# Performance work log

Measured on AMD Instinct MI355X. Metric: run time of the kernel, lower is better.

Reference implementation:

```python
import jax, jax.numpy as jnp
import numpy as np

D = 256; H = 8; HD = D // H; NK = 32; NLAYERS = 4; FF = 4 * D
B = 8; M = 768; N = 128; LT = 64; T = M + N + LT
SCALE = 1.0 / float(np.sqrt(HD))


def layer_norm(x, s, b):
    mu = x.mean(-1, keepdims=True)
    var = ((x - mu) ** 2).mean(-1, keepdims=True)
    return (x - mu) * jax.lax.rsqrt(var + 1e-5) * s + b


def sine_embed(pos, d):
    # MTR gen_sineembed_for_position: half dims for y, half for x, interleaved sin/cos
    half = d // 2
    dim_t = jnp.power(10000.0, 2.0 * (jnp.arange(half) // 2).astype(jnp.float32) / half)
    scale = 2.0 * np.pi
    def inter(e):
        return jnp.stack([jnp.sin(e[:, 0::2]), jnp.cos(e[:, 1::2])], -1).reshape(e.shape[0], -1)
    ex = pos[:, 0:1] * scale / dim_t
    ey = pos[:, 1:2] * scale / dim_t
    return jnp.concatenate([inter(ey), inter(ex)], -1)


def setup_inputs() -> dict:
    key = jax.random.key(0)
    ks = jax.random.split(key, 24)
    s = 0.02
    inp = {
        'map_token': jax.random.normal(ks[0], (B, M, D), jnp.float32),
        'agent_token': jax.random.normal(ks[1], (B, N, D), jnp.float32),
        'light_token': jax.random.normal(ks[2], (B, LT, D), jnp.float32),
        'map_position': jax.random.uniform(ks[3], (B, M, 2), jnp.float32) * 100.0,
        'agent_position': jax.random.uniform(ks[4], (B, N, 2), jnp.float32) * 100.0,
        'light_position': jax.random.uniform(ks[5], (B, LT, 2), jnp.float32) * 100.0,
        'map_valid_mask': jnp.ones((B, M), bool),
        'agent_valid_mask': jnp.ones((B, N), bool),
        'light_valid_mask': jnp.ones((B, LT), bool),
        'Wq': jax.random.normal(ks[6], (NLAYERS, D, D), jnp.float32) * s,
        'bq': jnp.zeros((NLAYERS, D), jnp.float32),
        'Wk': jax.random.normal(ks[7], (NLAYERS, D, D), jnp.float32) * s,
        'bk': jnp.zeros((NLAYERS, D), jnp.float32),
        'Wv': jax.random.normal(ks[8], (NLAYERS, D, D), jnp.float32) * s,
        'bv': jnp.zeros((NLAYERS, D), jnp.float32),
        'Wo': jax.random.normal(ks[9], (NLAYERS, D, D), jnp.float32) * s,
        'bo': jnp.zeros((NLAYERS, D), jnp.float32),
        'W1': jax.random.normal(ks[10], (NLAYERS, D, FF), jnp.float32) * s,
        'b1': jnp.zeros((NLAYERS, FF), jnp.float32),
        'W2': jax.random.normal(ks[11], (NLAYERS, FF, D), jnp.float32) * s,
        'b2': jnp.zeros((NLAYERS, D), jnp.float32),
        'ln1_s': jnp.ones((NLAYERS, D), jnp.float32),
        'ln1_b': jnp.zeros((NLAYERS, D), jnp.float32),
        'ln2_s': jnp.ones((NLAYERS, D), jnp.float32),
        'ln2_b': jnp.zeros((NLAYERS, D), jnp.float32),
    }
    return inp


def reference(map_token, agent_token, light_token, map_position, agent_position, light_position,
              map_valid_mask, agent_valid_mask, light_valid_mask,
              Wq, bq, Wk, bk, Wv, bv, Wo, bo, W1, b1, W2, b2, ln1_s, ln1_b, ln2_s, ln2_b):
    x = jnp.concatenate([map_token, agent_token, light_token], 1)             # [B,T,D]
    pos = jnp.concatenate([map_position, agent_position, light_position], 1)[..., :2]  # [B,T,2]
    # all tokens valid -> masked compaction is a static reshape
    xs = x.reshape(B * T, D)
    ps = pos.reshape(B * T, 2)
    # KNN within each scene (includes self, like knn_batch_mlogk on same set)
    d2 = jnp.sum((pos[:, :, None, :] - pos[:, None, :, :]) ** 2, -1)          # [B,T,T]
    _, idx = jax.lax.top_k(-d2, NK)                                            # [B,T,NK] local indices
    idx = (idx + (jnp.arange(B) * T)[:, None, None]).reshape(B * T, NK)        # global flat indices
    pe = sine_embed(ps, D)                                                     # [B*T,D]
    out = xs
    for l in range(NLAYERS):
        qk = out + pe
        q = (qk @ Wq[l] + bq[l]).reshape(-1, H, HD)
        k = (qk @ Wk[l] + bk[l]).reshape(-1, H, HD)
        v = (out @ Wv[l] + bv[l]).reshape(-1, H, HD)
        kn = k[idx]                                                            # [BT,NK,H,HD] gather
        vn = v[idx]
        att = jax.nn.softmax(jnp.einsum('nhd,nkhd->nhk', q, kn) * SCALE, axis=-1)
        a = jnp.einsum('nhk,nkhd->nhd', att, vn).reshape(-1, D) @ Wo[l] + bo[l]
        out = layer_norm(out + a, ln1_s[l], ln1_b[l])
        ff = jax.nn.relu(out @ W1[l] + b1[l]) @ W2[l] + b2[l]
        out = layer_norm(out + ff, ln2_s[l], ln2_b[l])
    full = out.reshape(B, T, D)
    return full[:, :M], full[:, M:M + N], full[:, M + N:]
```

## Files before the change

kernel.cpp:

```cpp
#include <hip/hip_runtime.h>
#include <math.h>

#define BB 8
#define MTOK 768
#define NTOK 128
#define LTOK 64
#define TT 960
#define BT 7680
#define DD 256
#define HH 8
#define HD 32
#define KNN 32
#define FFD 1024
#define NLAYERS 4
#define SCALE_ATT 0.17677669529663687f

typedef __attribute__((ext_vector_type(8))) short bfrag_t;
typedef __attribute__((ext_vector_type(4))) float accfrag_t;

__device__ __forceinline__ float b2f(unsigned short u) {
  union { unsigned int i; float f; } c; c.i = ((unsigned int)u) << 16; return c.f;
}
__device__ __forceinline__ unsigned short f2b(float f) {
  union { float f; unsigned int i; } c; c.f = f;
  return (unsigned short)((c.i + 0x7fffu + ((c.i >> 16) & 1u)) >> 16);
}
__device__ __forceinline__ float load_elem(const void* p, size_t i, int f) {
  return f ? b2f(((const unsigned short*)p)[i]) : ((const float*)p)[i];
}
__device__ __forceinline__ size_t pk_addr(int row, int col, int nks) {
  return ((size_t)((row >> 4) * nks + (col >> 5)) << 9)
       + (size_t)(((((col >> 3) & 3) << 4) + (row & 15)) * 8 + (col & 7));
}
__device__ __forceinline__ int swiz_tok(int blk) { return (blk & 7) * TT + (blk >> 3); }

__global__ __launch_bounds__(256)
void detect_kernel(const void* tok, int* flag) {
  __shared__ int cnt;
  if (threadIdx.x == 0) cnt = 0;
  __syncthreads();
  const unsigned short* u = (const unsigned short*)tok;
  int ok = 0;
  for (int i = threadIdx.x; i < 1024; i += 256) {
    int e = (u[i] >> 7) & 0xFF;
    if (e >= 100 && e <= 140) ok++;
  }
  atomicAdd(&cnt, ok);
  __syncthreads();
  if (threadIdx.x == 0) *flag = (cnt >= 922) ? 1 : 0;
}

#define FB_BQ 0
#define FB_BK 1024
#define FB_BV 2048
#define FB_BO 3072
#define FB_B1 4096
#define FB_B2 8192
#define FB_LN1S 9216
#define FB_LN1B 10240
#define FB_LN2S 11264
#define FB_LN2B 12288
#define FB_TOTAL 13312
struct ParamSrc { const void* p[13]; };
__global__ __launch_bounds__(256)
void conv_misc_kernel(ParamSrc ps, const int* flag, float* __restrict__ dst,
                      float* __restrict__ posf) {
  int f = *flag;
  if (blockIdx.x < BB) {
    int b = blockIdx.x;
    for (int t = threadIdx.x; t < TT * 2; t += 256) {
      int tok = t >> 1, c = t & 1;
      const void* p; size_t idx;
      if (tok < MTOK)             { p = ps.p[10]; idx = (size_t)(b * MTOK + tok) * 2 + c; }
      else if (tok < MTOK + NTOK) { p = ps.p[11]; idx = (size_t)(b * NTOK + tok - MTOK) * 2 + c; }
      else                        { p = ps.p[12]; idx = (size_t)(b * LTOK + tok - MTOK - NTOK) * 2 + c; }
      posf[((size_t)b * TT + tok) * 2 + c] = load_elem(p, idx, f);
    }
    return;
  }
  int i = (blockIdx.x - BB) * 256 + threadIdx.x;
  if (i >= FB_TOTAL) return;
  int src; size_t off;
  if (i < 4096)      { src = i >> 10;              off = i & 1023; }
  else if (i < 8192) { src = 4;                    off = i - 4096; }
  else               { src = 5 + ((i - 8192) >> 10); off = (i - 8192) & 1023; }
  dst[i] = load_elem(ps.p[src], off, f);
}

struct PackSrc { const void* s[6]; };
__global__ __launch_bounds__(256)
void packW_kernel(PackSrc w, const int* flag,
                  unsigned short* __restrict__ Wqkvpk, unsigned short* __restrict__ Wopk,
                  unsigned short* __restrict__ W1pk, unsigned short* __restrict__ W2pk) {
  int f = *flag;
  int id = blockIdx.x * 256 + threadIdx.x;
  const void* src; unsigned short* dst; int layer, e, K, N;
  if (id < 786432) {
    layer = id / 196608; int rest = id % 196608; int sel = rest / 65536; e = rest % 65536;
    src = w.s[sel]; dst = Wqkvpk + id; K = 256; N = 256;
  } else if (id < 1048576) {
    int off = id - 786432; layer = off / 65536; e = off % 65536;
    src = w.s[3]; dst = Wopk + off; K = 256; N = 256;
  } else if (id < 2097152) {
    int off = id - 1048576; layer = off / 262144; e = off % 262144;
    src = w.s[4]; dst = W1pk + off; K = 256; N = 1024;
  } else {
    int off = id - 2097152; layer = off / 262144; e = off % 262144;
    src = w.s[5]; dst = W2pk + off; K = 1024; N = 256;
  }
  int nks = K >> 5;
  int cb = e / (nks * 512);
  int ks = (e / 512) % nks;
  int lane = (e >> 3) & 63, j = e & 7;
  int col = cb * 16 + (lane & 15);
  int k = ks * 32 + (lane >> 4) * 8 + j;
  size_t si = (size_t)layer * K * N + (size_t)k * N + col;
  *dst = f ? ((const unsigned short*)src)[si] : f2b(((const float*)src)[si]);
}

__global__ __launch_bounds__(256)
void prep_kernel(const void* mt, const void* at, const void* lt,
                 const float* __restrict__ posf, const int* flag,
                 unsigned short* __restrict__ pe_b, float* __restrict__ out_f,
                 unsigned short* __restrict__ pk1, unsigned short* __restrict__ qkpk) {
  int n = swiz_tok(blockIdx.x), d = threadIdx.x;
  int b = n / TT, t = n - b * TT;
  int f = *flag;
  const void* src; size_t si;
  if (t < MTOK)              { src = mt; si = (size_t)(b * MTOK + t) * DD + d; }
  else if (t < MTOK + NTOK)  { src = at; si = (size_t)(b * NTOK + (t - MTOK)) * DD + d; }
  else                       { src = lt; si = (size_t)(b * LTOK + (t - MTOK - NTOK)) * DD + d; }
  float x = load_elem(src, si, f);
  float px = posf[((size_t)b * TT + t) * 2 + 0];
  float py = posf[((size_t)b * TT + t) * 2 + 1];
  float coord = (d < 128) ? py : px;
  int j = d & 127;
  float expo = (float)(2 * (j >> 1)) / 128.0f;
  float dim_t = powf(10000.0f, expo);
  float e = coord * 6.283185307179586f / dim_t;
  float p = (j & 1) ? cosf(e) : sinf(e);
  size_t o = (size_t)n * DD + d;
  pe_b[o] = f2b(p);
  out_f[o] = x;
  size_t pa = pk_addr(n, d, 8);
  pk1[pa] = f2b(x);
  qkpk[pa] = f2b(x + p);
}

__device__ __forceinline__ unsigned long long shfl_xor_u64(unsigned long long v, int m) {
  unsigned lo = (unsigned)v, hi = (unsigned)(v >> 32);
  lo = (unsigned)__shfl_xor((int)lo, m);
  hi = (unsigned)__shfl_xor((int)hi, m);
  return ((unsigned long long)hi << 32) | (unsigned long long)lo;
}
__device__ __forceinline__ unsigned long long shfl_u64(unsigned long long v, int srcLane) {
  unsigned lo = (unsigned)v, hi = (unsigned)(v >> 32);
  lo = (unsigned)__shfl((int)lo, srcLane);
  hi = (unsigned)__shfl((int)hi, srcLane);
  return ((unsigned long long)hi << 32) | (unsigned long long)lo;
}
__device__ __forceinline__ unsigned long long bitonic64(unsigned long long key, int lane) {
#pragma unroll
  for (int kk = 2; kk <= 64; kk <<= 1) {
#pragma unroll
    for (int j = kk >> 1; j > 0; j >>= 1) {
      unsigned long long other = shfl_xor_u64(key, j);
      bool small_ = (lane & j) == 0;
      bool dir = (lane & kk) == 0;
      bool keep = ((key < other) == (small_ == dir));
      key = keep ? key : other;
    }
  }
  return key;
}

__global__ __launch_bounds__(256)
void knn_kernel(const float* __restrict__ posf, int* __restrict__ idx_out) {
  __shared__ float sx[TT], sy[TT];
  __shared__ unsigned long long cbuf[4][64];
  int b = blockIdx.x & 7;
  int qbase = (blockIdx.x >> 3) * 4;
  for (int t = threadIdx.x; t < TT; t += 256) {
    sx[t] = posf[((size_t)b * TT + t) * 2 + 0];
    sy[t] = posf[((size_t)b * TT + t) * 2 + 1];
  }
  __syncthreads();
  int wave = threadIdx.x >> 6, lane = threadIdx.x & 63;
  int t = qbase + wave;
  float qx = sx[t], qy = sy[t];

  unsigned long long k[15];
#pragma unroll
  for (int c = 0; c < 15; c++) {
    int j = c * 64 + lane;
    float dx = qx - sx[j], dy = qy - sy[j];
    float d2 = __fadd_rn(__fmul_rn(dx, dx), __fmul_rn(dy, dy));
    k[c] = ((unsigned long long)__float_as_uint(d2) << 32) | (unsigned)j;
  }
  unsigned long long lm = k[0];
#pragma unroll
  for (int c = 1; c < 15; c++) lm = (k[c] < lm) ? k[c] : lm;

  unsigned long long sm = bitonic64(lm, lane);
  unsigned long long thr = shfl_u64(sm, 31);

  int c_l = 0;
#pragma unroll
  for (int c = 0; c < 15; c++) c_l += (k[c] <= thr) ? 1 : 0;
  int inc = c_l;
#pragma unroll
  for (int o = 1; o < 64; o <<= 1) {
    int tt = __shfl_up(inc, o);
    inc += (lane >= o) ? tt : 0;
  }
  int total = __shfl(inc, 63);
  int pos = inc - c_l;

  if (total <= 64) {
    unsigned long long* wb = cbuf[wave];
#pragma unroll
    for (int c = 0; c < 15; c++) {
      if (k[c] <= thr) { wb[pos] = k[c]; pos++; }
    }
    unsigned long long cand = (lane < total) ? wb[lane] : ~0ull;
    cand = bitonic64(cand, lane);
    if (lane < KNN)
      idx_out[((size_t)(b * TT + t)) * KNN + lane] = b * TT + (int)(cand & 0xFFFFFFFFu);
  } else {
    unsigned res = 0;
    for (int i = 0; i < KNN; i++) {
      unsigned long long m = k[0];
#pragma unroll
      for (int c = 1; c < 15; c++) m = (k[c] < m) ? k[c] : m;
#pragma unroll
      for (int o = 32; o > 0; o >>= 1) {
        unsigned long long om = shfl_xor_u64(m, o);
        m = (om < m) ? om : m;
      }
      if (lane == i) res = (unsigned)(m & 0xFFFFFFFFu);
      int owner = (int)(m & 63u), ch = (int)(((unsigned)(m & 0xFFFFFFFFu)) >> 6);
      if (lane == owner) {
#pragma unroll
        for (int c = 0; c < 15; c++) if (c == ch) k[c] = ~0ull;
      }
    }
    if (lane < KNN)
      idx_out[((size_t)(b * TT + t)) * KNN + lane] = b * TT + (int)res;
  }
}

template<int NKS>
__device__ __forceinline__ void wavegemm(const unsigned short* __restrict__ Apk,
                                         const unsigned short* __restrict__ Bpk,
                                         int rb, int cb0, accfrag_t (&acc)[4]) {
  const int lane = threadIdx.x & 63;
  accfrag_t z = {0.f, 0.f, 0.f, 0.f};
#pragma unroll
  for (int nt = 0; nt < 4; nt++) acc[nt] = z;
  const unsigned short* ap = Apk + ((size_t)rb * NKS * 512 + lane * 8);
  const unsigned short* bp = Bpk + ((size_t)cb0 * NKS * 512 + lane * 8);
#pragma unroll 4
  for (int ks = 0; ks < NKS; ks++) {
    bfrag_t a = *(const bfrag_t*)(ap + ks * 512);
#pragma unroll
    for (int nt = 0; nt < 4; nt++) {
      bfrag_t b = *(const bfrag_t*)(bp + (size_t)(nt * NKS + ks) * 512);
      acc[nt] = __builtin_amdgcn_mfma_f32_16x16x32_bf16(a, b, acc[nt], 0, 0, 0);
    }
  }
}

__global__ __launch_bounds__(256)
void qkv_kernel(const unsigned short* __restrict__ qkpk,
                const unsigned short* __restrict__ outpk,
                const unsigned short* __restrict__ Wl,
                const float* __restrict__ pb, int l,
                unsigned short* __restrict__ QKV) {
  int scene = blockIdx.x & 7, r = blockIdx.x >> 3;
  int rbg = r % 15, cgall = r / 15;
  int wave = threadIdx.x >> 6, lane = threadIdx.x & 63;
  int rb = scene * 60 + rbg * 4 + wave;
  int sel = cgall >> 2, cg = cgall & 3;
  const unsigned short* A = (sel < 2) ? qkpk : outpk;
  const unsigned short* B = Wl + sel * 65536;
  const float* bias = pb + sel * 1024 + l * 256;
  accfrag_t acc[4];
  wavegemm<8>(A, B, rb, cg * 4, acc);
  int l16 = lane & 15, lq = lane >> 4;
  unsigned short* C = QKV + (size_t)sel * BT * DD;
#pragma unroll
  for (int nt = 0; nt < 4; nt++) {
    int col = cg * 64 + nt * 16 + l16;
    float bv = bias[col];
#pragma unroll
    for (int r4 = 0; r4 < 4; r4++) {
      int row = rb * 16 + lq * 4 + r4;
      C[(size_t)row * DD + col] = f2b(acc[nt][r4] + bv);
    }
  }
}

__global__ __launch_bounds__(256)
void attn_kernel(const unsigned short* __restrict__ QKV,
                 const int* __restrict__ idx,
                 unsigned short* __restrict__ attnpk) {
  __shared__ unsigned short kn[KNN][DD + 8];
  __shared__ unsigned short vn[KNN][DD + 8];
  __shared__ float qs[DD];
  __shared__ float att[HH][KNN];
  __shared__ int nb[KNN];
  const unsigned short* Q = QKV;
  const unsigned short* K = QKV + (size_t)BT * DD;
  const unsigned short* V = QKV + 2 * (size_t)BT * DD;
  int n = swiz_tok(blockIdx.x), tid = threadIdx.x;
  if (tid < KNN) nb[tid] = idx[n * KNN + tid];
  qs[tid] = b2f(Q[(size_t)n * DD + tid]);
  __syncthreads();
#pragma unroll
  for (int p = 0; p < 4; p++) {
    int e = p * 256 + tid;
    int r = e >> 5, c8 = (e & 31) * 8;
    int srow = nb[r];
    *(uint4*)(&kn[r][c8]) = *(const uint4*)(K + (size_t)srow * DD + c8);
    *(uint4*)(&vn[r][c8]) = *(const uint4*)(V + (size_t)srow * DD + c8);
  }
  __syncthreads();
  int h = tid >> 5, kk = tid & 31;
  float dot = 0.0f;
#pragma unroll
  for (int d = 0; d < HD; d++) dot += qs[h * HD + d] * b2f(kn[kk][h * HD + d]);
  float sc = dot * SCALE_ATT;
  float mx = sc;
#pragma unroll
  for (int o = 16; o > 0; o >>= 1) mx = fmaxf(mx, __shfl_xor(mx, o, 32));
  float ex = expf(sc - mx);
  float sm = ex;
#pragma unroll
  for (int o = 16; o > 0; o >>= 1) sm += __shfl_xor(sm, o, 32);
  att[h][kk] = ex / sm;
  __syncthreads();
  int d = kk;
  float oacc = 0.0f;
#pragma unroll
  for (int k2 = 0; k2 < KNN; k2++) oacc += att[h][k2] * b2f(vn[k2][h * HD + d]);
  attnpk[pk_addr(n, tid, 8)] = f2b(oacc);
}

template<bool LAST>
__global__ __launch_bounds__(256)
void ffn_block_kernel(const unsigned short* __restrict__ attnpk,
                      const unsigned short* __restrict__ Wo,
                      const unsigned short* __restrict__ W1,
                      const unsigned short* __restrict__ W2,
                      const float* __restrict__ bo,
                      const float* __restrict__ b1,
                      const float* __restrict__ b2,
                      float* __restrict__ yf,
                      unsigned short* __restrict__ outpk, unsigned short* __restrict__ qkpk,
                      const unsigned short* __restrict__ pe_b,
                      const float* __restrict__ g1, const float* __restrict__ t1,
                      const float* __restrict__ g2, const float* __restrict__ t2,
                      void* __restrict__ dout, const int* __restrict__ flag) {
  __shared__ unsigned short xls[8 * 512];
  __shared__ unsigned short hls[32 * 512];
  __shared__ float ps1[4][16], ps2[4][16];
  int scene = blockIdx.x & 7, rbs = blockIdx.x >> 3;
  int wave = threadIdx.x >> 6, lane = threadIdx.x & 63;
  int rb = scene * 60 + rbs;
  int l16 = lane & 15, lq = lane >> 4;

  accfrag_t acc[4];
  wavegemm<8>(attnpk, Wo, rb, wave * 4, acc);
  float y[4][4];
  float s[4] = {0.f, 0.f, 0.f, 0.f}, s2[4] = {0.f, 0.f, 0.f, 0.f};
#pragma unroll
  for (int nt = 0; nt < 4; nt++) {
    int col = wave * 64 + nt * 16 + l16;
    float bv = bo[col];
#pragma unroll
    for (int r4 = 0; r4 < 4; r4++) {
      int row = rb * 16 + lq * 4 + r4;
      float x = acc[nt][r4] + bv + yf[(size_t)row * DD + col];
      y[nt][r4] = x; s[r4] += x; s2[r4] += x * x;
    }
  }
#pragma unroll
  for (int o = 1; o < 16; o <<= 1) {
#pragma unroll
    for (int r4 = 0; r4 < 4; r4++) { s[r4] += __shfl_xor(s[r4], o); s2[r4] += __shfl_xor(s2[r4], o); }
  }
  if (l16 == 0) {
#pragma unroll
    for (int r4 = 0; r4 < 4; r4++) { ps1[wave][lq * 4 + r4] = s[r4]; ps2[wave][lq * 4 + r4] = s2[r4]; }
  }
  __syncthreads();
#pragma unroll
  for (int r4 = 0; r4 < 4; r4++) {
    int r16 = lq * 4 + r4;
    float ts  = ps1[0][r16] + ps1[1][r16] + ps1[2][r16] + ps1[3][r16];
    float ts2 = ps2[0][r16] + ps2[1][r16] + ps2[2][r16] + ps2[3][r16];
    float mu = ts * (1.0f / 256.0f);
    float var = ts2 * (1.0f / 256.0f) - mu * mu;
    float rstd = 1.0f / sqrtf(fmaxf(var, 0.f) + 1e-5f);
#pragma unroll
    for (int nt = 0; nt < 4; nt++) {
      int col = wave * 64 + nt * 16 + l16;
      float v = (y[nt][r4] - mu) * rstd * g1[col] + t1[col];
      y[nt][r4] = v;
      xls[pk_addr(r16, col, 8)] = f2b(v);
    }
  }
  __syncthreads();

#pragma unroll
  for (int i = 0; i < 4; i++) {
    int cg = wave * 4 + i;
    accfrag_t a2[4];
    wavegemm<8>(xls, W1, 0, cg * 4, a2);
#pragma unroll
    for (int nt = 0; nt < 4; nt++) {
      int col = cg * 64 + nt * 16 + l16;
      float bv = b1[col];
#pragma unroll
      for (int r4 = 0; r4 < 4; r4++)
        hls[pk_addr(lq * 4 + r4, col, 32)] = f2b(fmaxf(a2[nt][r4] + bv, 0.0f));
    }
  }
  __syncthreads();

  accfrag_t a3[4];
  wavegemm<32>(hls, W2, 0, wave * 4, a3);
  float v2[4][4];
  float s3[4] = {0.f, 0.f, 0.f, 0.f}, s4[4] = {0.f, 0.f, 0.f, 0.f};
#pragma unroll
  for (int nt = 0; nt < 4; nt++) {
    int col = wave * 64 + nt * 16 + l16;
    float bv = b2[col];
#pragma unroll
    for (int r4 = 0; r4 < 4; r4++) {
      float x = a3[nt][r4] + bv + y[nt][r4];
      v2[nt][r4] = x; s3[r4] += x; s4[r4] += x * x;
    }
  }
#pragma unroll
  for (int o = 1; o < 16; o <<= 1) {
#pragma unroll
    for (int r4 = 0; r4 < 4; r4++) { s3[r4] += __shfl_xor(s3[r4], o); s4[r4] += __shfl_xor(s4[r4], o); }
  }
  if (l16 == 0) {
#pragma unroll
    for (int r4 = 0; r4 < 4; r4++) { ps1[wave][lq * 4 + r4] = s3[r4]; ps2[wave][lq * 4 + r4] = s4[r4]; }
  }
  __syncthreads();
  int fl = LAST ? *flag : 0;
#pragma unroll
  for (int r4 = 0; r4 < 4; r4++) {
    int r16 = lq * 4 + r4;
    float ts  = ps1[0][r16] + ps1[1][r16] + ps1[2][r16] + ps1[3][r16];
    float ts2 = ps2[0][r16] + ps2[1][r16] + ps2[2][r16] + ps2[3][r16];
    float mu = ts * (1.0f / 256.0f);
    float var = ts2 * (1.0f / 256.0f) - mu * mu;
    float rstd = 1.0f / sqrtf(fmaxf(var, 0.f) + 1e-5f);
#pragma unroll
    for (int nt = 0; nt < 4; nt++) {
      int col = wave * 64 + nt * 16 + l16;
      float yv = (v2[nt][r4] - mu) * rstd * g2[col] + t2[col];
      int row = rb * 16 + r16;
      if (!LAST) {
        yf[(size_t)row * DD + col] = yv;
        outpk[pk_addr(row, col, 8)] = f2b(yv);
        float q = yv + b2f(pe_b[(size_t)row * DD + col]);
        qkpk[pk_addr(row, col, 8)] = f2b(q);
      } else {
        int t = rbs * 16 + r16;
        size_t o;
        if (t < MTOK)             o = (size_t)(scene * MTOK + t) * DD + col;
        else if (t < MTOK + NTOK) o = (size_t)BB * MTOK * DD + (size_t)(scene * NTOK + (t - MTOK)) * DD + col;
        else                      o = (size_t)BB * MTOK * DD + (size_t)BB * NTOK * DD
                                    + (size_t)(scene * LTOK + (t - MTOK - NTOK)) * DD + col;
        if (fl) ((unsigned short*)dout)[o] = f2b(yv);
        else    ((float*)dout)[o] = yv;
      }
    }
  }
}

extern "C" void kernel_launch(void* const* d_in, const int* in_sizes, int n_in,
                              void* d_out, int out_size, void* d_ws, size_t ws_size,
                              hipStream_t stream) {
  const void* map_tok   = d_in[0];
  const void* agent_tok = d_in[1];
  const void* light_tok = d_in[2];
  const void* map_pos   = d_in[3];
  const void* agent_pos = d_in[4];
  const void* light_pos = d_in[5];
  const void* Wq  = d_in[9];
  const void* bq  = d_in[10];
  const void* Wk  = d_in[11];
  const void* bk  = d_in[12];
  const void* Wv  = d_in[13];
  const void* bv  = d_in[14];
  const void* Wo  = d_in[15];
  const void* bo  = d_in[16];
  const void* W1  = d_in[17];
  const void* b1  = d_in[18];
  const void* W2  = d_in[19];
  const void* b2  = d_in[20];
  const void* ln1s = d_in[21];
  const void* ln1b = d_in[22];
  const void* ln2s = d_in[23];
  const void* ln2b = d_in[24];

  size_t off = 0;
  char* base = (char*)d_ws;
  auto take = [&](size_t bytes) { char* p = base + off; off += (bytes + 255) & ~(size_t)255; return (void*)p; };
  int*   flag  = (int*)take(256);
  float* posf  = (float*)take((size_t)BT * 2 * 4);
  float* pbuf  = (float*)take((size_t)FB_TOTAL * 4);
  unsigned short* pe_b = (unsigned short*)take((size_t)BT * DD * 2);
  float* out_f = (float*)take((size_t)BT * DD * 4);
  unsigned short* pk1  = (unsigned short*)take((size_t)BT * DD * 2);
  unsigned short* qkpk = (unsigned short*)take((size_t)BT * DD * 2);
  unsigned short* QKV  = (unsigned short*)take((size_t)3 * BT * DD * 2);
  unsigned short* attnpk = (unsigned short*)take((size_t)BT * DD * 2);
  int* idxb = (int*)take((size_t)BT * KNN * 4);
  unsigned short* Wqkvpk = (unsigned short*)take((size_t)NLAYERS * 3 * DD * DD * 2);
  unsigned short* Wopk   = (unsigned short*)take((size_t)NLAYERS * DD * DD * 2);
  unsigned short* W1pk   = (unsigned short*)take((size_t)NLAYERS * DD * FFD * 2);
  unsigned short* W2pk   = (unsigned short*)take((size_t)NLAYERS * DD * FFD * 2);

  detect_kernel<<<1, 256, 0, stream>>>(map_tok, flag);
  ParamSrc ps; ps.p[0]=bq; ps.p[1]=bk; ps.p[2]=bv; ps.p[3]=bo; ps.p[4]=b1;
  ps.p[5]=b2; ps.p[6]=ln1s; ps.p[7]=ln1b; ps.p[8]=ln2s; ps.p[9]=ln2b;
  ps.p[10]=map_pos; ps.p[11]=agent_pos; ps.p[12]=light_pos;
  conv_misc_kernel<<<BB + (FB_TOTAL + 255) / 256, 256, 0, stream>>>(ps, flag, pbuf, posf);

  PackSrc pw; pw.s[0]=Wq; pw.s[1]=Wk; pw.s[2]=Wv; pw.s[3]=Wo; pw.s[4]=W1; pw.s[5]=W2;
  packW_kernel<<<12288, 256, 0, stream>>>(pw, flag, Wqkvpk, Wopk, W1pk, W2pk);

  prep_kernel<<<BT, 256, 0, stream>>>(map_tok, agent_tok, light_tok, posf, flag,
                                      pe_b, out_f, pk1, qkpk);
  knn_kernel<<<1920, 256, 0, stream>>>(posf, idxb);

  for (int l = 0; l < NLAYERS; l++) {
    qkv_kernel<<<1440, 256, 0, stream>>>(qkpk, pk1, Wqkvpk + (size_t)l * 3 * 65536,
                                         pbuf, l, QKV);
    attn_kernel<<<BT, 256, 0, stream>>>(QKV, idxb, attnpk);
    if (l < NLAYERS - 1)
      ffn_block_kernel<false><<<480, 256, 0, stream>>>(
          attnpk, Wopk + (size_t)l * 65536, W1pk + (size_t)l * 262144, W2pk + (size_t)l * 262144,
          pbuf + FB_BO + l * 256, pbuf + FB_B1 + l * 1024, pbuf + FB_B2 + l * 256,
          out_f, pk1, qkpk, pe_b,
          pbuf + FB_LN1S + l * 256, pbuf + FB_LN1B + l * 256,
          pbuf + FB_LN2S + l * 256, pbuf + FB_LN2B + l * 256,
          d_out, flag);
    else
      ffn_block_kernel<true><<<480, 256, 0, stream>>>(
          attnpk, Wopk + (size_t)l * 65536, W1pk + (size_t)l * 262144, W2pk + (size_t)l * 262144,
          pbuf + FB_BO + l * 256, pbuf + FB_B1 + l * 1024, pbuf + FB_B2 + l * 256,
          out_f, pk1, qkpk, pe_b,
          pbuf + FB_LN1S + l * 256, pbuf + FB_LN1B + l * 256,
          pbuf + FB_LN2S + l * 256, pbuf + FB_LN2B + l * 256,
          d_out, flag);
  }
}
```

Baseline: 429.9 us.

## Fuse next-layer QKV projection into FFN block and merge setup kernels

Folds the detect step into conv_misc and merges packW, prep and knn into one launch using block-index ranges. Weight packing now reads the source coalesced and scatters into the packed layout. The FFN block keeps its normalized output tile in shared memory and computes the next layer's Q/K/V projection in place. This removes the separate per-layer qkv launch and the round trip of pk1/qkpk through global memory. The cost is more per-block work and shared-memory reuse in the FFN kernel, which may lower occupancy.

```diff
diff --git a/kernel.cpp b/kernel.cpp
--- a/kernel.cpp
+++ b/kernel.cpp
@@ -34,22 +34,6 @@
 }
 __device__ __forceinline__ int swiz_tok(int blk) { return (blk & 7) * TT + (blk >> 3); }
 
-__global__ __launch_bounds__(256)
-void detect_kernel(const void* tok, int* flag) {
-  __shared__ int cnt;
-  if (threadIdx.x == 0) cnt = 0;
-  __syncthreads();
-  const unsigned short* u = (const unsigned short*)tok;
-  int ok = 0;
-  for (int i = threadIdx.x; i < 1024; i += 256) {
-    int e = (u[i] >> 7) & 0xFF;
-    if (e >= 100 && e <= 140) ok++;
-  }
-  atomicAdd(&cnt, ok);
-  __syncthreads();
-  if (threadIdx.x == 0) *flag = (cnt >= 922) ? 1 : 0;
-}
-
 #define FB_BQ 0
 #define FB_BK 1024
 #define FB_BV 2048
@@ -63,18 +47,30 @@
 #define FB_TOTAL 13312
 struct ParamSrc { const void* p[13]; };
 __global__ __launch_bounds__(256)
-void conv_misc_kernel(ParamSrc ps, const int* flag, float* __restrict__ dst,
-                      float* __restrict__ posf) {
-  int f = *flag;
+void conv_misc_kernel(ParamSrc ps, const void* tok, int* flagout,
+                      float* __restrict__ dst, float* __restrict__ posf) {
+  __shared__ int cnt;
+  if (threadIdx.x == 0) cnt = 0;
+  __syncthreads();
+  const unsigned short* u = (const unsigned short*)tok;
+  int ok = 0;
+  for (int i = threadIdx.x; i < 1024; i += 256) {
+    int e = (u[i] >> 7) & 0xFF;
+    if (e >= 100 && e <= 140) ok++;
+  }
+  atomicAdd(&cnt, ok);
+  __syncthreads();
+  int f = (cnt >= 922) ? 1 : 0;
+  if (blockIdx.x == 0 && threadIdx.x == 0) *flagout = f;
   if (blockIdx.x < BB) {
     int b = blockIdx.x;
     for (int t = threadIdx.x; t < TT * 2; t += 256) {
-      int tok = t >> 1, c = t & 1;
+      int tok2 = t >> 1, c = t & 1;
       const void* p; size_t idx;
-      if (tok < MTOK)             { p = ps.p[10]; idx = (size_t)(b * MTOK + tok) * 2 + c; }
-      else if (tok < MTOK + NTOK) { p = ps.p[11]; idx = (size_t)(b * NTOK + tok - MTOK) * 2 + c; }
-      else                        { p = ps.p[12]; idx = (size_t)(b * LTOK + tok - MTOK - NTOK) * 2 + c; }
-      posf[((size_t)b * TT + tok) * 2 + c] = load_elem(p, idx, f);
+      if (tok2 < MTOK)             { p = ps.p[10]; idx = (size_t)(b * MTOK + tok2) * 2 + c; }
+      else if (tok2 < MTOK + NTOK) { p = ps.p[11]; idx = (size_t)(b * NTOK + tok2 - MTOK) * 2 + c; }
+      else                         { p = ps.p[12]; idx = (size_t)(b * LTOK + tok2 - MTOK - NTOK) * 2 + c; }
+      posf[((size_t)b * TT + tok2) * 2 + c] = load_elem(p, idx, f);
     }
     return;
   }
@@ -87,66 +83,6 @@
   dst[i] = load_elem(ps.p[src], off, f);
 }
 
-struct PackSrc { const void* s[6]; };
-__global__ __launch_bounds__(256)
-void packW_kernel(PackSrc w, const int* flag,
-                  unsigned short* __restrict__ Wqkvpk, unsigned short* __restrict__ Wopk,
-                  unsigned short* __restrict__ W1pk, unsigned short* __restrict__ W2pk) {
-  int f = *flag;
-  int id = blockIdx.x * 256 + threadIdx.x;
-  const void* src; unsigned short* dst; int layer, e, K, N;
-  if (id < 786432) {
-    layer = id / 196608; int rest = id % 196608; int sel = rest / 65536; e = rest % 65536;
-    src = w.s[sel]; dst = Wqkvpk + id; K = 256; N = 256;
-  } else if (id < 1048576) {
-    int off = id - 786432; layer = off / 65536; e = off % 65536;
-    src = w.s[3]; dst = Wopk + off; K = 256; N = 256;
-  } else if (id < 2097152) {
-    int off = id - 1048576; layer = off / 262144; e = off % 262144;
-    src = w.s[4]; dst = W1pk + off; K = 256; N = 1024;
-  } else {
-    int off = id - 2097152; layer = off / 262144; e = off % 262144;
-    src = w.s[5]; dst = W2pk + off; K = 1024; N = 256;
-  }
-  int nks = K >> 5;
-  int cb = e / (nks * 512);
-  int ks = (e / 512) % nks;
-  int lane = (e >> 3) & 63, j = e & 7;
-  int col = cb * 16 + (lane & 15);
-  int k = ks * 32 + (lane >> 4) * 8 + j;
-  size_t si = (size_t)layer * K * N + (size_t)k * N + col;
-  *dst = f ? ((const unsigned short*)src)[si] : f2b(((const float*)src)[si]);
-}
-
-__global__ __launch_bounds__(256)
-void prep_kernel(const void* mt, const void* at, const void* lt,
-                 const float* __restrict__ posf, const int* flag,
-                 unsigned short* __restrict__ pe_b, float* __restrict__ out_f,
-                 unsigned short* __restrict__ pk1, unsigned short* __restrict__ qkpk) {
-  int n = swiz_tok(blockIdx.x), d = threadIdx.x;
-  int b = n / TT, t = n - b * TT;
-  int f = *flag;
-  const void* src; size_t si;
-  if (t < MTOK)              { src = mt; si = (size_t)(b * MTOK + t) * DD + d; }
-  else if (t < MTOK + NTOK)  { src = at; si = (size_t)(b * NTOK + (t - MTOK)) * DD + d; }
-  else                       { src = lt; si = (size_t)(b * LTOK + (t - MTOK - NTOK)) * DD + d; }
-  float x = load_elem(src, si, f);
-  float px = posf[((size_t)b * TT + t) * 2 + 0];
-  float py = posf[((size_t)b * TT + t) * 2 + 1];
-  float coord = (d < 128) ? py : px;
-  int j = d & 127;
-  float expo = (float)(2 * (j >> 1)) / 128.0f;
-  float dim_t = powf(10000.0f, expo);
-  float e = coord * 6.283185307179586f / dim_t;
-  float p = (j & 1) ? cosf(e) : sinf(e);
-  size_t o = (size_t)n * DD + d;
-  pe_b[o] = f2b(p);
-  out_f[o] = x;
-  size_t pa = pk_addr(n, d, 8);
-  pk1[pa] = f2b(x);
-  qkpk[pa] = f2b(x + p);
-}
-
 __device__ __forceinline__ unsigned long long shfl_xor_u64(unsigned long long v, int m) {
   unsigned lo = (unsigned)v, hi = (unsigned)(v >> 32);
   lo = (unsigned)__shfl_xor((int)lo, m);
@@ -174,12 +110,78 @@
   return key;
 }
 
+struct PackSrc { const void* s[6]; };
 __global__ __launch_bounds__(256)
-void knn_kernel(const float* __restrict__ posf, int* __restrict__ idx_out) {
+void mega_kernel(PackSrc w, const void* mt, const void* at, const void* lt,
+                 const float* __restrict__ posf, const int* __restrict__ flag,
+                 unsigned short* __restrict__ Wqkvpk, unsigned short* __restrict__ Wopk,
+                 unsigned short* __restrict__ W1pk, unsigned short* __restrict__ W2pk,
+                 unsigned short* __restrict__ pe_b, float* __restrict__ out_f,
+                 unsigned short* __restrict__ pk1, unsigned short* __restrict__ qkpk,
+                 int* __restrict__ idx_out) {
   __shared__ float sx[TT], sy[TT];
   __shared__ unsigned long long cbuf[4][64];
-  int b = blockIdx.x & 7;
-  int qbase = (blockIdx.x >> 3) * 4;
+  int bid = blockIdx.x;
+  if (bid < 12288) {
+    int f = *flag;
+    int id = bid * 256 + threadIdx.x;
+    if (id < 786432) {
+      int layer = id / 196608, rest = id % 196608;
+      int sel = rest >> 16, e = rest & 65535;
+      int k = e >> 8, col = e & 255;
+      const void* src = w.s[sel];
+      size_t si = (size_t)layer * 65536 + e;
+      Wqkvpk[(size_t)layer * 196608 + (size_t)sel * 65536 + pk_addr(col, k, 8)] =
+          f ? ((const unsigned short*)src)[si] : f2b(((const float*)src)[si]);
+    } else if (id < 1048576) {
+      int off = id - 786432, layer = off >> 16, e = off & 65535;
+      int k = e >> 8, col = e & 255;
+      size_t si = (size_t)layer * 65536 + e;
+      Wopk[(size_t)layer * 65536 + pk_addr(col, k, 8)] =
+          f ? ((const unsigned short*)w.s[3])[si] : f2b(((const float*)w.s[3])[si]);
+    } else if (id < 2097152) {
+      int off = id - 1048576, layer = off >> 18, e = off & 262143;
+      int k = e >> 10, col = e & 1023;
+      size_t si = (size_t)layer * 262144 + e;
+      W1pk[(size_t)layer * 262144 + pk_addr(col, k, 8)] =
+          f ? ((const unsigned short*)w.s[4])[si] : f2b(((const float*)w.s[4])[si]);
+    } else {
+      int off = id - 2097152, layer = off >> 18, e = off & 262143;
+      int k = e >> 8, col = e & 255;
+      size_t si = (size_t)layer * 262144 + e;
+      W2pk[(size_t)layer * 262144 + pk_addr(col, k, 32)] =
+          f ? ((const unsigned short*)w.s[5])[si] : f2b(((const float*)w.s[5])[si]);
+    }
+    return;
+  }
+  if (bid < 19968) {
+    int n = swiz_tok(bid - 12288), d = threadIdx.x;
+    int b = n / TT, t = n - b * TT;
+    int f = *flag;
+    const void* src; size_t si;
+    if (t < MTOK)              { src = mt; si = (size_t)(b * MTOK + t) * DD + d; }
+    else if (t < MTOK + NTOK)  { src = at; si = (size_t)(b * NTOK + (t - MTOK)) * DD + d; }
+    else                       { src = lt; si = (size_t)(b * LTOK + (t - MTOK - NTOK)) * DD + d; }
+    float x = load_elem(src, si, f);
+    float px = posf[((size_t)b * TT + t) * 2 + 0];
+    float py = posf[((size_t)b * TT + t) * 2 + 1];
+    float coord = (d < 128) ? py : px;
+    int j = d & 127;
+    float expo = (float)(2 * (j >> 1)) / 128.0f;
+    float dim_t = powf(10000.0f, expo);
+    float e = coord * 6.283185307179586f / dim_t;
+    float p = (j & 1) ? cosf(e) : sinf(e);
+    size_t o = (size_t)n * DD + d;
+    pe_b[o] = f2b(p);
+    out_f[o] = x;
+    size_t pa = pk_addr(n, d, 8);
+    pk1[pa] = f2b(x);
+    qkpk[pa] = f2b(x + p);
+    return;
+  }
+  int kb = bid - 19968;
+  int b = kb & 7;
+  int qbase = (kb >> 3) * 4;
   for (int t = threadIdx.x; t < TT; t += 256) {
     sx[t] = posf[((size_t)b * TT + t) * 2 + 0];
     sy[t] = posf[((size_t)b * TT + t) * 2 + 1];
@@ -352,14 +354,16 @@
                       const unsigned short* __restrict__ Wo,
                       const unsigned short* __restrict__ W1,
                       const unsigned short* __restrict__ W2,
+                      const unsigned short* __restrict__ Wn,
                       const float* __restrict__ bo,
                       const float* __restrict__ b1,
                       const float* __restrict__ b2,
+                      const float* __restrict__ pb, int ln,
                       float* __restrict__ yf,
-                      unsigned short* __restrict__ outpk, unsigned short* __restrict__ qkpk,
                       const unsigned short* __restrict__ pe_b,
                       const float* __restrict__ g1, const float* __restrict__ t1,
                       const float* __restrict__ g2, const float* __restrict__ t2,
+                      unsigned short* __restrict__ QKV,
                       void* __restrict__ dout, const int* __restrict__ flag) {
   __shared__ unsigned short xls[8 * 512];
   __shared__ unsigned short hls[32 * 512];
@@ -452,6 +456,7 @@
     for (int r4 = 0; r4 < 4; r4++) { ps1[wave][lq * 4 + r4] = s3[r4]; ps2[wave][lq * 4 + r4] = s4[r4]; }
   }
   __syncthreads();
+  unsigned short* qkls = hls;
   int fl = LAST ? *flag : 0;
 #pragma unroll
   for (int r4 = 0; r4 < 4; r4++) {
@@ -468,9 +473,9 @@
       int row = rb * 16 + r16;
       if (!LAST) {
         yf[(size_t)row * DD + col] = yv;
-        outpk[pk_addr(row, col, 8)] = f2b(yv);
         float q = yv + b2f(pe_b[(size_t)row * DD + col]);
-        qkpk[pk_addr(row, col, 8)] = f2b(q);
+        xls[pk_addr(r16, col, 8)] = f2b(yv);
+        qkls[pk_addr(r16, col, 8)] = f2b(q);
       } else {
         int t = rbs * 16 + r16;
         size_t o;
@@ -480,6 +485,30 @@
                                     + (size_t)(scene * LTOK + (t - MTOK - NTOK)) * DD + col;
         if (fl) ((unsigned short*)dout)[o] = f2b(yv);
         else    ((float*)dout)[o] = yv;
+      }
+    }
+  }
+
+  if (!LAST) {
+    __syncthreads();
+#pragma unroll
+    for (int i = 0; i < 3; i++) {
+      int cgall = wave * 3 + i;
+      int sel = cgall >> 2, cg = cgall & 3;
+      const unsigned short* A = (sel < 2) ? qkls : xls;
+      accfrag_t a4[4];
+      wavegemm<8>(A, Wn + sel * 65536, 0, cg * 4, a4);
+      const float* bias = pb + sel * 1024 + ln * 256;
+      unsigned short* C = QKV + (size_t)sel * BT * DD;
+#pragma unroll
+      for (int nt = 0; nt < 4; nt++) {
+        int col = cg * 64 + nt * 16 + l16;
+        float bv = bias[col];
+#pragma unroll
+        for (int r4 = 0; r4 < 4; r4++) {
+          int row = rb * 16 + lq * 4 + r4;
+          C[(size_t)row * DD + col] = f2b(a4[nt][r4] + bv);
+        }
       }
     }
   }
@@ -529,38 +558,39 @@
   unsigned short* W1pk   = (unsigned short*)take((size_t)NLAYERS * DD * FFD * 2);
   unsigned short* W2pk   = (unsigned short*)take((size_t)NLAYERS * DD * FFD * 2);
 
-  detect_kernel<<<1, 256, 0, stream>>>(map_tok, flag);
   ParamSrc ps; ps.p[0]=bq; ps.p[1]=bk; ps.p[2]=bv; ps.p[3]=bo; ps.p[4]=b1;
   ps.p[5]=b2; ps.p[6]=ln1s; ps.p[7]=ln1b; ps.p[8]=ln2s; ps.p[9]=ln2b;
   ps.p[10]=map_pos; ps.p[11]=agent_pos; ps.p[12]=light_pos;
-  conv_misc_kernel<<<BB + (FB_TOTAL + 255) / 256, 256, 0, stream>>>(ps, flag, pbuf, posf);
+  conv_misc_kernel<<<BB + (FB_TOTAL + 255) / 256, 256, 0, stream>>>(ps, map_tok, flag, pbuf, posf);
 
   PackSrc pw; pw.s[0]=Wq; pw.s[1]=Wk; pw.s[2]=Wv; pw.s[3]=Wo; pw.s[4]=W1; pw.s[5]=W2;
-  packW_kernel<<<12288, 256, 0, stream>>>(pw, flag, Wqkvpk, Wopk, W1pk, W2pk);
-
-  prep_kernel<<<BT, 256, 0, stream>>>(map_tok, agent_tok, light_tok, posf, flag,
-                                      pe_b, out_f, pk1, qkpk);
-  knn_kernel<<<1920, 256, 0, stream>>>(posf, idxb);
+  mega_kernel<<<21888, 256, 0, stream>>>(pw, map_tok, agent_tok, light_tok, posf, flag,
+                                         Wqkvpk, Wopk, W1pk, W2pk,
+                                         pe_b, out_f, pk1, qkpk, idxb);
+
+  qkv_kernel<<<1440, 256, 0, stream>>>(qkpk, pk1, Wqkvpk, pbuf, 0, QKV);
 
   for (int l = 0; l < NLAYERS; l++) {
-    qkv_kernel<<<1440, 256, 0, stream>>>(qkpk, pk1, Wqkvpk + (size_t)l * 3 * 65536,
-                                         pbuf, l, QKV);
     attn_kernel<<<BT, 256, 0, stream>>>(QKV, idxb, attnpk);
     if (l < NLAYERS - 1)
       ffn_block_kernel<false><<<480, 256, 0, stream>>>(
           attnpk, Wopk + (size_t)l * 65536, W1pk + (size_t)l * 262144, W2pk + (size_t)l * 262144,
+          Wqkvpk + (size_t)(l + 1) * 196608,
           pbuf + FB_BO + l * 256, pbuf + FB_B1 + l * 1024, pbuf + FB_B2 + l * 256,
-          out_f, pk1, qkpk, pe_b,
+          pbuf, l + 1,
+          out_f, pe_b,
           pbuf + FB_LN1S + l * 256, pbuf + FB_LN1B + l * 256,
           pbuf + FB_LN2S + l * 256, pbuf + FB_LN2B + l * 256,
-          d_out, flag);
+          QKV, d_out, flag);
     else
       ffn_block_kernel<true><<<480, 256, 0, stream>>>(
           attnpk, Wopk + (size_t)l * 65536, W1pk + (size_t)l * 262144, W2pk + (size_t)l * 262144,
+          Wqkvpk,
           pbuf + FB_BO + l * 256, pbuf + FB_B1 + l * 1024, pbuf + FB_B2 + l * 256,
-          out_f, pk1, qkpk, pe_b,
+          pbuf, 0,
+          out_f, pe_b,
           pbuf + FB_LN1S + l * 256, pbuf + FB_LN1B + l * 256,
           pbuf + FB_LN2S + l * 256, pbuf + FB_LN2B + l * 256,
-          d_out, flag);
-  }
-}
+          QKV, d_out, flag);
+  }
+}
```

Result: faster. 409.3 us (-4.8%).
